# Performance work log

Hardware: AMD Instinct MI355X
Metric: run time of the kernel (lower is better)

The kernel has to match this reference:

```python
import jax, jax.numpy as jnp
import numpy as np

B, S, D, H = 2, 2048, 1024, 16
DK = D // H


def setup_inputs() -> dict:
    key = jax.random.key(0)
    ks = jax.random.split(key, 14)
    inp = {
        'query': jax.random.normal(ks[0], (B, S, D), jnp.float32),
        'key': jax.random.normal(ks[1], (B, S, D), jnp.float32),
        'value': jax.random.normal(ks[2], (B, S, D), jnp.float32),
        'mask': jax.random.randint(ks[3], (B, 1, S, S), 0, 2).astype(bool),
        'rel_pos_bias': jax.random.normal(ks[4], (1, H, S, S), jnp.float32),
    }
    scale = 1.0 / np.sqrt(D)
    names = ['Wq', 'bq', 'Wk', 'bk', 'Wv', 'bv', 'Wo', 'bo']
    for i, n in enumerate(names):
        k = ks[5 + i]
        if n.startswith('W'):
            inp[n] = jax.random.normal(k, (D, D), jnp.float32) * scale
        else:
            inp[n] = jnp.zeros((D,), jnp.float32)
    return inp


def reference(query, key, value, mask, rel_pos_bias, Wq, bq, Wk, bk, Wv, bv, Wo, bo):
    # torch Linear: y = x @ W^T + b; W stored [out, in]
    def proj(x, W, b):
        y = x @ W.T + b                       # [B,S,D]
        return y.reshape(B, S, H, DK).transpose(0, 2, 1, 3)  # [B,H,S,DK]

    q = proj(query, Wq, bq)
    k = proj(key, Wk, bk)
    v = proj(value, Wv, bv)

    scores = jnp.einsum('bhqd,bhkd->bhqk', q, k) / jnp.sqrt(jnp.float32(DK))
    scores = scores + rel_pos_bias
    scores = jnp.where(mask, jnp.float32(-1e9), scores)
    p_attn = jax.nn.softmax(scores, axis=-1)
    x = jnp.einsum('bhqk,bhkd->bhqd', p_attn, v)  # [B,H,S,DK]
    x = x.transpose(0, 2, 1, 3).reshape(B, S, D)
    return x @ Wo.T + bo
```

## Files before the change

### kernel.cpp

```cpp
#include <hip/hip_runtime.h>
#include <stdint.h>


typedef _Float16 f16;
typedef _Float16 f16x8 __attribute__((ext_vector_type(8)));
typedef _Float16 f16x4 __attribute__((ext_vector_type(4)));
typedef __fp16 h2 __attribute__((ext_vector_type(2)));
typedef float f32x4 __attribute__((ext_vector_type(4)));

#define LOG2E 1.44269504088896340736f

__device__ __forceinline__ void gload16(const void* g, void* l) {
  __builtin_amdgcn_global_load_lds(
      (const __attribute__((address_space(1))) unsigned int*)g,
      (__attribute__((address_space(3))) unsigned int*)l, 16, 0, 0);
}

struct CvtSrcs { const float* s[7]; };

__global__ __launch_bounds__(256) void cvt_all(CvtSrcs a, f16* __restrict__ out) {
  const int i = blockIdx.x * 256 + threadIdx.x;
  int r, base;
  if (i < 3145728) { r = i >> 20; base = r << 20; }
  else { r = 3 + ((i - 3145728) >> 18); base = 3145728 + ((r - 3) << 18); }
  const float4 v = ((const float4*)a.s[r])[i - base];
  f16x4 o = {(f16)v.x, (f16)v.y, (f16)v.z, (f16)v.w};
  ((f16x4*)out)[i] = o;
}

__global__ void mask_detect(const uint8_t* __restrict__ m, int* __restrict__ flag) {
  __shared__ int s_off, s_weird;
  const int t = threadIdx.x;
  if (t == 0) { s_off = 0; s_weird = 0; }
  __syncthreads();
  int f_off = 0, f_weird = 0;
  for (int i = t; i < 8192; i += 256) {
    const uint8_t v = m[i];
    if ((i & 3) && v) f_off = 1;
    if (v > 1) f_weird = 1;
  }
  if (f_off) atomicOr(&s_off, 1);
  if (f_weird) atomicOr(&s_weird, 1);
  __syncthreads();
  if (t == 0) *flag = (s_off && !s_weird) ? 1 : 0;
}

__global__ __launch_bounds__(256) void mask_canon(const uint8_t* __restrict__ m,
                                                  uint8_t* __restrict__ out,
                                                  const int* __restrict__ flag) {
  const int i = (blockIdx.x * 256 + threadIdx.x) * 4;
  uchar4 o;
  if (*flag) {
    const uchar4 v = *(const uchar4*)(m + i);
    o = make_uchar4(v.x != 0, v.y != 0, v.z != 0, v.w != 0);
  } else {
    const int4 v = *(const int4*)((const int*)m + i);
    o = make_uchar4(v.x != 0, v.y != 0, v.z != 0, v.w != 0);
  }
  *(uchar4*)(out + i) = o;
}

__global__ __launch_bounds__(256, 2) void gemm_qkv(
    const f16* __restrict__ qh, const f16* __restrict__ kh, const f16* __restrict__ vh,
    const f16* __restrict__ wq, const f16* __restrict__ wk, const f16* __restrict__ wv,
    const float* __restrict__ bq, const float* __restrict__ bk, const float* __restrict__ bv,
    f16* __restrict__ Qp, f16* __restrict__ Kp, f16* __restrict__ Vt) {
  constexpr int K = 1024;
  const int t = threadIdx.x;
  const int w = t >> 6, lane = t & 63, l15 = lane & 15, l4 = lane >> 4;
  const int nt = (int)blockIdx.x % 48;
  const int bm = ((int)blockIdx.x / 48) * 128;
  const int which = nt >> 4;
  const int bn = (nt & 15) * 64;
  const f16* A = which == 0 ? qh : which == 1 ? kh : vh;
  const f16* Bw = which == 0 ? wq : which == 1 ? wk : wv;
  const float* bias = which == 0 ? bq : which == 1 ? bk : bv;

  __shared__ f16 As[2][128 * 32];
  __shared__ f16 Bs[2][64 * 32];

  const f16* a0 = A + (size_t)(bm + (t >> 2)) * K + (t & 3) * 8;
  const f16* a1 = a0 + (size_t)64 * K;
  const f16* b0 = Bw + (size_t)(bn + (t >> 2)) * K + (t & 3) * 8;

  f32x4 acc[2][4];
#pragma unroll
  for (int m = 0; m < 2; ++m)
#pragma unroll
    for (int n = 0; n < 4; ++n) acc[m][n] = (f32x4){0.f, 0.f, 0.f, 0.f};

#define STAGE_G(buf, k0)                          \
  do {                                            \
    gload16(a0 + (k0), &As[buf][w * 512]);        \
    gload16(a1 + (k0), &As[buf][2048 + w * 512]); \
    gload16(b0 + (k0), &Bs[buf][w * 512]);        \
  } while (0)

  STAGE_G(0, 0);
  __syncthreads();
  int cur = 0;
#pragma unroll 1
  for (int kt = 0; kt < 32; ++kt) {
    if (kt < 31) STAGE_G(cur ^ 1, (kt + 1) * 32);
    const f16* ap = &As[cur][(w * 32 + l15) * 32 + l4 * 8];
    const f16* bp = &Bs[cur][l15 * 32 + l4 * 8];
    f16x8 af[2], bfr[4];
#pragma unroll
    for (int m = 0; m < 2; ++m) af[m] = *(const f16x8*)(ap + m * 512);
#pragma unroll
    for (int n = 0; n < 4; ++n) bfr[n] = *(const f16x8*)(bp + n * 512);
#pragma unroll
    for (int m = 0; m < 2; ++m)
#pragma unroll
      for (int n = 0; n < 4; ++n)
        acc[m][n] = __builtin_amdgcn_mfma_f32_16x16x32_f16(af[m], bfr[n], acc[m][n], 0, 0, 0);
    __syncthreads();
    cur ^= 1;
  }
#undef STAGE_G

  const float scale = which == 0 ? 0.125f * LOG2E : 1.0f;
  f16* outp = which == 0 ? Qp : which == 1 ? Kp : Vt;
#pragma unroll
  for (int m = 0; m < 2; ++m) {
    const int r0 = bm + w * 32 + m * 16 + (l4 << 2);
#pragma unroll
    for (int n = 0; n < 4; ++n) {
      const int c = bn + n * 16 + l15;
      const float bv = bias[c];
#pragma unroll
      for (int j = 0; j < 4; ++j) {
        const int r = r0 + j;
        const float v = (acc[m][n][j] + bv) * scale;
        const int b_ = r >> 11, s = r & 2047, h_ = c >> 6, dk = c & 63;
        if (which < 2)
          outp[(((size_t)b_ * 16 + h_) * 2048 + s) * 64 + dk] = (f16)v;
        else
          outp[(((size_t)b_ * 16 + h_) * 64 + dk) * 2048 + s] = (f16)v;
      }
    }
  }
}

__global__ __launch_bounds__(256, 2) void gemm_out(const f16* __restrict__ A,
                                                   const f16* __restrict__ Bw,
                                                   const float* __restrict__ bias,
                                                   float* __restrict__ outp) {
  constexpr int K = 1024;
  const int t = threadIdx.x;
  const int w = t >> 6, lane = t & 63, l15 = lane & 15, l4 = lane >> 4;
  const int bm = (int)(blockIdx.x >> 4) * 128;
  const int bn = (int)(blockIdx.x & 15) * 64;

  __shared__ f16 As[2][128 * 32];
  __shared__ f16 Bs[2][64 * 32];

  const f16* a0 = A + (size_t)(bm + (t >> 2)) * K + (t & 3) * 8;
  const f16* a1 = a0 + (size_t)64 * K;
  const f16* b0 = Bw + (size_t)(bn + (t >> 2)) * K + (t & 3) * 8;

  f32x4 acc[2][4];
#pragma unroll
  for (int m = 0; m < 2; ++m)
#pragma unroll
    for (int n = 0; n < 4; ++n) acc[m][n] = (f32x4){0.f, 0.f, 0.f, 0.f};

#define STAGE_G(buf, k0)                          \
  do {                                            \
    gload16(a0 + (k0), &As[buf][w * 512]);        \
    gload16(a1 + (k0), &As[buf][2048 + w * 512]); \
    gload16(b0 + (k0), &Bs[buf][w * 512]);        \
  } while (0)

  STAGE_G(0, 0);
  __syncthreads();
  int cur = 0;
#pragma unroll 1
  for (int kt = 0; kt < 32; ++kt) {
    if (kt < 31) STAGE_G(cur ^ 1, (kt + 1) * 32);
    const f16* ap = &As[cur][(w * 32 + l15) * 32 + l4 * 8];
    const f16* bp = &Bs[cur][l15 * 32 + l4 * 8];
    f16x8 af[2], bfr[4];
#pragma unroll
    for (int m = 0; m < 2; ++m) af[m] = *(const f16x8*)(ap + m * 512);
#pragma unroll
    for (int n = 0; n < 4; ++n) bfr[n] = *(const f16x8*)(bp + n * 512);
#pragma unroll
    for (int m = 0; m < 2; ++m)
#pragma unroll
      for (int n = 0; n < 4; ++n)
        acc[m][n] = __builtin_amdgcn_mfma_f32_16x16x32_f16(af[m], bfr[n], acc[m][n], 0, 0, 0);
    __syncthreads();
    cur ^= 1;
  }
#undef STAGE_G

#pragma unroll
  for (int m = 0; m < 2; ++m) {
    const int r0 = bm + w * 32 + m * 16 + (l4 << 2);
#pragma unroll
    for (int n = 0; n < 4; ++n) {
      const int c = bn + n * 16 + l15;
      const float bv = bias[c];
#pragma unroll
      for (int j = 0; j < 4; ++j)
        outp[(size_t)(r0 + j) * 1024 + c] = acc[m][n][j] + bv;
    }
  }
}

__device__ __forceinline__ const f16x8* swzr(const f16* base, int row, int bytecol) {
  return (const f16x8*)((const char*)base + row * 128 + (bytecol ^ ((row & 7) << 4)));
}

__global__ __launch_bounds__(256, 2) void attn_fwd(
    const f16* __restrict__ Qp, const f16* __restrict__ Kp,
    const f16* __restrict__ Vt, const float* __restrict__ bias,
    const uint8_t* __restrict__ mask, f16* __restrict__ X) {
  constexpr int S = 2048;
  const int bid = blockIdx.x;
  const int sb = (bid & 7) * 64 + (bid >> 3);
  const int qt = sb & 31, h = sb >> 5;
  const int t = threadIdx.x, w = t >> 6, lane = t & 63;
  const int l15 = lane & 15, l4 = lane >> 4;
  const int q0 = qt * 64 + w * 16;

  const f16* Qb[2] = {Qp + (size_t)h * S * 64, Qp + (size_t)(16 + h) * S * 64};
  const f16* Kb[2] = {Kp + (size_t)h * S * 64, Kp + (size_t)(16 + h) * S * 64};
  const f16* Vb[2] = {Vt + (size_t)h * 64 * S, Vt + (size_t)(16 + h) * 64 * S};
  const float* biasr = bias + (size_t)h * S * S + (size_t)(q0 + l15) * S + l4 * 4;
  const uint8_t* mr0 = mask + (size_t)(q0 + l15) * S + l4 * 4;
  const uint8_t* mr1 = mr0 + (size_t)S * S;

  __shared__ f16 Ks[2][2][64 * 64];
  __shared__ f16 Vs[2][2][64 * 64];
  __shared__ f16 Ps[4][16 * 64];

  f16x8 qf[2][2];
#pragma unroll
  for (int bb = 0; bb < 2; ++bb)
#pragma unroll
    for (int ks = 0; ks < 2; ++ks)
      qf[bb][ks] =
          *(const f16x8*)(Qb[bb] + (size_t)(q0 + l15) * 64 + ks * 32 + l4 * 8);

  f32x4 oacc[2][4];
#pragma unroll
  for (int bb = 0; bb < 2; ++bb)
#pragma unroll
    for (int n = 0; n < 4; ++n) oacc[bb][n] = (f32x4){0.f, 0.f, 0.f, 0.f};
  float mrow[2] = {-3e38f, -3e38f}, lrow[2] = {0.f, 0.f};

  f32x4 bc[2][4];
  uint32_t mc[2][2][4];

  const int srow = t >> 3;
  const int scol = (((t & 7) ^ (srow & 7)) << 3);

#define STAGE(bf, kk)                                                                    \
  do {                                                                                   \
    gload16(Kb[0] + (size_t)((kk) + srow) * 64 + scol, &Ks[bf][0][w * 512]);             \
    gload16(Kb[0] + (size_t)((kk) + 32 + srow) * 64 + scol, &Ks[bf][0][2048 + w * 512]); \
    gload16(Kb[1] + (size_t)((kk) + srow) * 64 + scol, &Ks[bf][1][w * 512]);             \
    gload16(Kb[1] + (size_t)((kk) + 32 + srow) * 64 + scol, &Ks[bf][1][2048 + w * 512]); \
    gload16(Vb[0] + (size_t)srow * S + (kk) + scol, &Vs[bf][0][w * 512]);                \
    gload16(Vb[0] + (size_t)(32 + srow) * S + (kk) + scol, &Vs[bf][0][2048 + w * 512]);  \
    gload16(Vb[1] + (size_t)srow * S + (kk) + scol, &Vs[bf][1][w * 512]);                \
    gload16(Vb[1] + (size_t)(32 + srow) * S + (kk) + scol, &Vs[bf][1][2048 + w * 512]);  \
  } while (0)

#define LOADB(SET, kk)                                      \
  do {                                                      \
    bc[SET][0] = *(const f32x4*)(biasr + (kk));             \
    bc[SET][1] = *(const f32x4*)(biasr + (kk) + 16);        \
    bc[SET][2] = *(const f32x4*)(biasr + (kk) + 32);        \
    bc[SET][3] = *(const f32x4*)(biasr + (kk) + 48);        \
    mc[SET][0][0] = *(const uint32_t*)(mr0 + (kk));         \
    mc[SET][0][1] = *(const uint32_t*)(mr0 + (kk) + 16);    \
    mc[SET][0][2] = *(const uint32_t*)(mr0 + (kk) + 32);    \
    mc[SET][0][3] = *(const uint32_t*)(mr0 + (kk) + 48);    \
    mc[SET][1][0] = *(const uint32_t*)(mr1 + (kk));         \
    mc[SET][1][1] = *(const uint32_t*)(mr1 + (kk) + 16);    \
    mc[SET][1][2] = *(const uint32_t*)(mr1 + (kk) + 32);    \
    mc[SET][1][3] = *(const uint32_t*)(mr1 + (kk) + 48);    \
  } while (0)

#define TILE(BUF, SET, KNEXT)                                                            \
  do {                                                                                   \
    asm volatile("s_waitcnt vmcnt(20)" ::: "memory");                                    \
    __builtin_amdgcn_s_barrier();                                                        \
    asm volatile("" ::: "memory");                                                       \
    f32x4 sacc[2][4];                                                                    \
    _Pragma("unroll") for (int bb = 0; bb < 2; ++bb)                                     \
      _Pragma("unroll") for (int n = 0; n < 4; ++n)                                      \
        sacc[bb][n] = (f32x4){0.f, 0.f, 0.f, 0.f};                                       \
    _Pragma("unroll") for (int bb = 0; bb < 2; ++bb)                                     \
      _Pragma("unroll") for (int n = 0; n < 4; ++n)                                      \
        _Pragma("unroll") for (int ks = 0; ks < 2; ++ks) {                               \
          const f16x8 kf = *swzr(&Ks[BUF][bb][0], n * 16 + l15, ks * 64 + l4 * 16);      \
          sacc[bb][n] = __builtin_amdgcn_mfma_f32_16x16x32_f16(kf, qf[bb][ks],           \
                                                               sacc[bb][n], 0, 0, 0);    \
        }                                                                                \
    _Pragma("unroll") for (int bb = 0; bb < 2; ++bb) {                                   \
      float tmax = -3e38f;                                                               \
      _Pragma("unroll") for (int n = 0; n < 4; ++n) {                                    \
        _Pragma("unroll") for (int j = 0; j < 4; ++j) {                                  \
          const float mf = (float)((mc[SET][bb][n] >> (8 * j)) & 255u);                  \
          sacc[bb][n][j] =                                                               \
              fmaf(mf, -2e9f, fmaf(bc[SET][n][j], LOG2E, sacc[bb][n][j]));               \
        }                                                                                \
        tmax = fmaxf(tmax, fmaxf(fmaxf(sacc[bb][n][0], sacc[bb][n][1]),                  \
                                 fmaxf(sacc[bb][n][2], sacc[bb][n][3])));                \
      }                                                                                  \
      tmax = fmaxf(tmax, __shfl_xor(tmax, 16));                                          \
      tmax = fmaxf(tmax, __shfl_xor(tmax, 32));                                          \
      const float mnew = fmaxf(mrow[bb], tmax);                                          \
      const float alpha = __builtin_exp2f(mrow[bb] - mnew);                              \
      mrow[bb] = mnew;                                                                   \
      float lsum = 0.f;                                                                  \
      _Pragma("unroll") for (int n = 0; n < 4; ++n)                                      \
        _Pragma("unroll") for (int j = 0; j < 4; ++j) {                                  \
          const float e = __builtin_exp2f(sacc[bb][n][j] - mnew);                        \
          sacc[bb][n][j] = e;                                                            \
          lsum += e;                                                                     \
        }                                                                                \
      lsum += __shfl_xor(lsum, 16);                                                      \
      lsum += __shfl_xor(lsum, 32);                                                      \
      lrow[bb] = lrow[bb] * alpha + lsum;                                                \
      float aq[4];                                                                       \
      _Pragma("unroll") for (int j = 0; j < 4; ++j) aq[j] = __shfl(alpha, l4 * 4 + j);   \
      _Pragma("unroll") for (int n = 0; n < 4; ++n)                                      \
        _Pragma("unroll") for (int j = 0; j < 4; ++j) oacc[bb][n][j] *= aq[j];           \
      _Pragma("unroll") for (int n = 0; n < 4; ++n) {                                    \
        h2 p01 = __builtin_amdgcn_cvt_pkrtz(sacc[bb][n][0], sacc[bb][n][1]);             \
        h2 p23 = __builtin_amdgcn_cvt_pkrtz(sacc[bb][n][2], sacc[bb][n][3]);             \
        f16x4 pk;                                                                        \
        pk[0] = (f16)p01[0]; pk[1] = (f16)p01[1];                                        \
        pk[2] = (f16)p23[0]; pk[3] = (f16)p23[1];                                        \
        *(f16x4*)((char*)&Ps[w][0] + l15 * 128 +                                         \
                  ((32 * n + 8 * l4) ^ ((l15 & 7) << 4))) = pk;                          \
      }                                                                                  \
      f16x8 pf[2];                                                                       \
      _Pragma("unroll") for (int ks = 0; ks < 2; ++ks)                                   \
        pf[ks] = *swzr(&Ps[w][0], l15, ks * 64 + l4 * 16);                               \
      _Pragma("unroll") for (int ks = 0; ks < 2; ++ks)                                   \
        _Pragma("unroll") for (int n = 0; n < 4; ++n) {                                  \
          const f16x8 vf = *swzr(&Vs[BUF][bb][0], n * 16 + l15, ks * 64 + l4 * 16);      \
          oacc[bb][n] = __builtin_amdgcn_mfma_f32_16x16x32_f16(pf[ks], vf,               \
                                                               oacc[bb][n], 0, 0, 0);    \
        }                                                                                \
    }                                                                                    \
    __builtin_amdgcn_s_barrier();                                                        \
    asm volatile("" ::: "memory");                                                       \
    STAGE(BUF, KNEXT);                                                                   \
    LOADB(SET, KNEXT);                                                                   \
  } while (0)

  STAGE(0, 0);
  LOADB(0, 0);
  STAGE(1, 64);
  LOADB(1, 64);

#pragma unroll 1
  for (int kt = 0; kt < 32; kt += 2) {
    TILE(0, 0, ((kt + 2) * 64) & (S - 1));
    TILE(1, 1, ((kt + 3) * 64) & (S - 1));
  }
#undef TILE
#undef LOADB
#undef STAGE

  asm volatile("s_waitcnt vmcnt(0)" ::: "memory");

#pragma unroll
  for (int bb = 0; bb < 2; ++bb) {
    const float inv = 1.0f / lrow[bb];
    float invq[4];
#pragma unroll
    for (int j = 0; j < 4; ++j) invq[j] = __shfl(inv, l4 * 4 + j);
#pragma unroll
    for (int j = 0; j < 4; ++j) {
      const int qrow = q0 + l4 * 4 + j;
#pragma unroll
      for (int n = 0; n < 4; ++n)
        X[((size_t)bb * 2048 + qrow) * 1024 + h * 64 + n * 16 + l15] =
            (f16)(oacc[bb][n][j] * invq[j]);
    }
  }
}

extern "C" void kernel_launch(void* const* d_in, const int* in_sizes, int n_in,
                              void* d_out, int out_size, void* d_ws, size_t ws_size,
                              hipStream_t stream) {
  const float* query = (const float*)d_in[0];
  const float* key_ = (const float*)d_in[1];
  const float* value = (const float*)d_in[2];
  const uint8_t* mask = (const uint8_t*)d_in[3];
  const float* bias = (const float*)d_in[4];
  const float* Wq = (const float*)d_in[5];
  const float* bq = (const float*)d_in[6];
  const float* Wk = (const float*)d_in[7];
  const float* bk = (const float*)d_in[8];
  const float* Wv = (const float*)d_in[9];
  const float* bv = (const float*)d_in[10];
  const float* Wo = (const float*)d_in[11];
  const float* bo = (const float*)d_in[12];

  char* p = (char*)d_ws;
  f16* qh = (f16*)p; p += (size_t)4194304 * 2;
  f16* kh = (f16*)p; p += (size_t)4194304 * 2;
  f16* vh = (f16*)p; p += (size_t)4194304 * 2;
  f16* wqh = (f16*)p; p += (size_t)1048576 * 2;
  f16* wkh = (f16*)p; p += (size_t)1048576 * 2;
  f16* wvh = (f16*)p; p += (size_t)1048576 * 2;
  f16* woh = (f16*)p; p += (size_t)1048576 * 2;
  f16* Qp = (f16*)p; p += (size_t)4194304 * 2;
  f16* Kp = (f16*)p; p += (size_t)4194304 * 2;
  f16* Vt = (f16*)p; p += (size_t)4194304 * 2;
  f16* Xh = (f16*)p; p += (size_t)4194304 * 2;
  uint8_t* m8 = (uint8_t*)p; p += (size_t)8388608;
  int* flag = (int*)p; p += 256;
  if (ws_size < (size_t)(p - (char*)d_ws)) return;

  mask_detect<<<1, 256, 0, stream>>>(mask, flag);
  mask_canon<<<8192, 256, 0, stream>>>(mask, m8, flag);

  CvtSrcs cs;
  cs.s[0] = query; cs.s[1] = key_; cs.s[2] = value;
  cs.s[3] = Wq; cs.s[4] = Wk; cs.s[5] = Wv; cs.s[6] = Wo;
  cvt_all<<<16384, 256, 0, stream>>>(cs, qh);

  gemm_qkv<<<1536, 256, 0, stream>>>(qh, kh, vh, wqh, wkh, wvh, bq, bk, bv,
                                     Qp, Kp, Vt);

  attn_fwd<<<512, 256, 0, stream>>>(Qp, Kp, Vt, bias, m8, Xh);

  gemm_out<<<512, 256, 0, stream>>>(Xh, woh, bo, (float*)d_out);
}
```

Baseline: 273.0 us.

## Load K/V MFMA fragments directly from global memory instead of LDS staging

Drops the double-buffered LDS staging of K and V tiles, the async global-to-LDS loads and the block barriers. Each wave now reads its MFMA operand fragments for K and V straight from global memory, relying on L1/L2 to serve the reuse across the four waves. The bias and mask prefetch is turned into a simple register ping-pong issued one tile ahead, and the swizzled block-to-head mapping is replaced by a linear one. This removes barrier sync and LDS traffic, but each wave issues four times the global K/V loads and their latency is no longer hidden by the LDS pipeline.

```diff
diff --git a/kernel.cpp b/kernel.cpp
--- a/kernel.cpp
+++ b/kernel.cpp
@@ -209,31 +209,26 @@
   }
 }
 
-__device__ __forceinline__ const f16x8* swzr(const f16* base, int row, int bytecol) {
-  return (const f16x8*)((const char*)base + row * 128 + (bytecol ^ ((row & 7) << 4)));
-}
-
 __global__ __launch_bounds__(256, 2) void attn_fwd(
     const f16* __restrict__ Qp, const f16* __restrict__ Kp,
     const f16* __restrict__ Vt, const float* __restrict__ bias,
     const uint8_t* __restrict__ mask, f16* __restrict__ X) {
   constexpr int S = 2048;
   const int bid = blockIdx.x;
-  const int sb = (bid & 7) * 64 + (bid >> 3);
-  const int qt = sb & 31, h = sb >> 5;
+  const int qt = bid & 31, h = bid >> 5;
   const int t = threadIdx.x, w = t >> 6, lane = t & 63;
   const int l15 = lane & 15, l4 = lane >> 4;
   const int q0 = qt * 64 + w * 16;
 
   const f16* Qb[2] = {Qp + (size_t)h * S * 64, Qp + (size_t)(16 + h) * S * 64};
-  const f16* Kb[2] = {Kp + (size_t)h * S * 64, Kp + (size_t)(16 + h) * S * 64};
-  const f16* Vb[2] = {Vt + (size_t)h * 64 * S, Vt + (size_t)(16 + h) * 64 * S};
+  const f16* kf0 = Kp + (size_t)h * S * 64 + (size_t)l15 * 64 + l4 * 8;
+  const f16* kf1 = kf0 + (size_t)16 * S * 64;
+  const f16* vf0 = Vt + (size_t)h * 64 * S + (size_t)l15 * S + l4 * 8;
+  const f16* vf1 = vf0 + (size_t)16 * 64 * S;
   const float* biasr = bias + (size_t)h * S * S + (size_t)(q0 + l15) * S + l4 * 4;
   const uint8_t* mr0 = mask + (size_t)(q0 + l15) * S + l4 * 4;
   const uint8_t* mr1 = mr0 + (size_t)S * S;
 
-  __shared__ f16 Ks[2][2][64 * 64];
-  __shared__ f16 Vs[2][2][64 * 64];
   __shared__ f16 Ps[4][16 * 64];
 
   f16x8 qf[2][2];
@@ -251,63 +246,40 @@
     for (int n = 0; n < 4; ++n) oacc[bb][n] = (f32x4){0.f, 0.f, 0.f, 0.f};
   float mrow[2] = {-3e38f, -3e38f}, lrow[2] = {0.f, 0.f};
 
-  f32x4 bc[2][4];
-  uint32_t mc[2][2][4];
-
-  const int srow = t >> 3;
-  const int scol = (((t & 7) ^ (srow & 7)) << 3);
-
-#define STAGE(bf, kk)                                                                    \
+  f32x4 bcA[4], bcB[4];
+  uint32_t mcA[2][4], mcB[2][4];
+
+#define LOADB(BC, MC, kk)                                   \
+  do {                                                      \
+    _Pragma("unroll") for (int n = 0; n < 4; ++n) {         \
+      BC[n] = *(const f32x4*)(biasr + (kk) + n * 16);       \
+      MC[0][n] = *(const uint32_t*)(mr0 + (kk) + n * 16);   \
+      MC[1][n] = *(const uint32_t*)(mr1 + (kk) + n * 16);   \
+    }                                                       \
+  } while (0)
+
+#define TILE(BC, MC, BCN, MCN, k0)                                                       \
   do {                                                                                   \
-    gload16(Kb[0] + (size_t)((kk) + srow) * 64 + scol, &Ks[bf][0][w * 512]);             \
-    gload16(Kb[0] + (size_t)((kk) + 32 + srow) * 64 + scol, &Ks[bf][0][2048 + w * 512]); \
-    gload16(Kb[1] + (size_t)((kk) + srow) * 64 + scol, &Ks[bf][1][w * 512]);             \
-    gload16(Kb[1] + (size_t)((kk) + 32 + srow) * 64 + scol, &Ks[bf][1][2048 + w * 512]); \
-    gload16(Vb[0] + (size_t)srow * S + (kk) + scol, &Vs[bf][0][w * 512]);                \
-    gload16(Vb[0] + (size_t)(32 + srow) * S + (kk) + scol, &Vs[bf][0][2048 + w * 512]);  \
-    gload16(Vb[1] + (size_t)srow * S + (kk) + scol, &Vs[bf][1][w * 512]);                \
-    gload16(Vb[1] + (size_t)(32 + srow) * S + (kk) + scol, &Vs[bf][1][2048 + w * 512]);  \
-  } while (0)
-
-#define LOADB(SET, kk)                                      \
-  do {                                                      \
-    bc[SET][0] = *(const f32x4*)(biasr + (kk));             \
-    bc[SET][1] = *(const f32x4*)(biasr + (kk) + 16);        \
-    bc[SET][2] = *(const f32x4*)(biasr + (kk) + 32);        \
-    bc[SET][3] = *(const f32x4*)(biasr + (kk) + 48);        \
-    mc[SET][0][0] = *(const uint32_t*)(mr0 + (kk));         \
-    mc[SET][0][1] = *(const uint32_t*)(mr0 + (kk) + 16);    \
-    mc[SET][0][2] = *(const uint32_t*)(mr0 + (kk) + 32);    \
-    mc[SET][0][3] = *(const uint32_t*)(mr0 + (kk) + 48);    \
-    mc[SET][1][0] = *(const uint32_t*)(mr1 + (kk));         \
-    mc[SET][1][1] = *(const uint32_t*)(mr1 + (kk) + 16);    \
-    mc[SET][1][2] = *(const uint32_t*)(mr1 + (kk) + 32);    \
-    mc[SET][1][3] = *(const uint32_t*)(mr1 + (kk) + 48);    \
-  } while (0)
-
-#define TILE(BUF, SET, KNEXT)                                                            \
-  do {                                                                                   \
-    asm volatile("s_waitcnt vmcnt(20)" ::: "memory");                                    \
-    __builtin_amdgcn_s_barrier();                                                        \
-    asm volatile("" ::: "memory");                                                       \
+    LOADB(BCN, MCN, ((k0) + 64) & (S - 1));                                              \
     f32x4 sacc[2][4];                                                                    \
     _Pragma("unroll") for (int bb = 0; bb < 2; ++bb)                                     \
       _Pragma("unroll") for (int n = 0; n < 4; ++n)                                      \
         sacc[bb][n] = (f32x4){0.f, 0.f, 0.f, 0.f};                                       \
-    _Pragma("unroll") for (int bb = 0; bb < 2; ++bb)                                     \
-      _Pragma("unroll") for (int n = 0; n < 4; ++n)                                      \
-        _Pragma("unroll") for (int ks = 0; ks < 2; ++ks) {                               \
-          const f16x8 kf = *swzr(&Ks[BUF][bb][0], n * 16 + l15, ks * 64 + l4 * 16);      \
-          sacc[bb][n] = __builtin_amdgcn_mfma_f32_16x16x32_f16(kf, qf[bb][ks],           \
-                                                               sacc[bb][n], 0, 0, 0);    \
-        }                                                                                \
+    _Pragma("unroll") for (int n = 0; n < 4; ++n)                                        \
+      _Pragma("unroll") for (int ks = 0; ks < 2; ++ks) {                                 \
+        const f16x8 k0f = *(const f16x8*)(kf0 + (size_t)((k0) + n * 16) * 64 + ks * 32); \
+        const f16x8 k1f = *(const f16x8*)(kf1 + (size_t)((k0) + n * 16) * 64 + ks * 32); \
+        sacc[0][n] = __builtin_amdgcn_mfma_f32_16x16x32_f16(k0f, qf[0][ks],              \
+                                                            sacc[0][n], 0, 0, 0);        \
+        sacc[1][n] = __builtin_amdgcn_mfma_f32_16x16x32_f16(k1f, qf[1][ks],              \
+                                                            sacc[1][n], 0, 0, 0);        \
+      }                                                                                  \
     _Pragma("unroll") for (int bb = 0; bb < 2; ++bb) {                                   \
       float tmax = -3e38f;                                                               \
       _Pragma("unroll") for (int n = 0; n < 4; ++n) {                                    \
         _Pragma("unroll") for (int j = 0; j < 4; ++j) {                                  \
-          const float mf = (float)((mc[SET][bb][n] >> (8 * j)) & 255u);                  \
-          sacc[bb][n][j] =                                                               \
-              fmaf(mf, -2e9f, fmaf(bc[SET][n][j], LOG2E, sacc[bb][n][j]));               \
+          const float mf = (float)((MC[bb][n] >> (8 * j)) & 255u);                       \
+          sacc[bb][n][j] = fmaf(mf, -2e9f, fmaf(BC[n][j], LOG2E, sacc[bb][n][j]));       \
         }                                                                                \
         tmax = fmaxf(tmax, fmaxf(fmaxf(sacc[bb][n][0], sacc[bb][n][1]),                  \
                                  fmaxf(sacc[bb][n][2], sacc[bb][n][3])));                \
@@ -342,35 +314,28 @@
       }                                                                                  \
       f16x8 pf[2];                                                                       \
       _Pragma("unroll") for (int ks = 0; ks < 2; ++ks)                                   \
-        pf[ks] = *swzr(&Ps[w][0], l15, ks * 64 + l4 * 16);                               \
+        pf[ks] = *(const f16x8*)((const char*)&Ps[w][0] + l15 * 128 +                    \
+                                 ((ks * 64 + l4 * 16) ^ ((l15 & 7) << 4)));              \
+      const f16* vfb = (bb == 0) ? vf0 : vf1;                                            \
       _Pragma("unroll") for (int ks = 0; ks < 2; ++ks)                                   \
         _Pragma("unroll") for (int n = 0; n < 4; ++n) {                                  \
-          const f16x8 vf = *swzr(&Vs[BUF][bb][0], n * 16 + l15, ks * 64 + l4 * 16);      \
+          const f16x8 vf =                                                               \
+              *(const f16x8*)(vfb + (size_t)n * 16 * S + (k0) + ks * 32);                \
           oacc[bb][n] = __builtin_amdgcn_mfma_f32_16x16x32_f16(pf[ks], vf,               \
                                                                oacc[bb][n], 0, 0, 0);    \
         }                                                                                \
     }                                                                                    \
-    __builtin_amdgcn_s_barrier();                                                        \
-    asm volatile("" ::: "memory");                                                       \
-    STAGE(BUF, KNEXT);                                                                   \
-    LOADB(SET, KNEXT);                                                                   \
   } while (0)
 
-  STAGE(0, 0);
-  LOADB(0, 0);
-  STAGE(1, 64);
-  LOADB(1, 64);
+  LOADB(bcA, mcA, 0);
 
 #pragma unroll 1
   for (int kt = 0; kt < 32; kt += 2) {
-    TILE(0, 0, ((kt + 2) * 64) & (S - 1));
-    TILE(1, 1, ((kt + 3) * 64) & (S - 1));
+    TILE(bcA, mcA, bcB, mcB, kt * 64);
+    TILE(bcB, mcB, bcA, mcA, (kt + 1) * 64);
   }
 #undef TILE
 #undef LOADB
-#undef STAGE
-
-  asm volatile("s_waitcnt vmcnt(0)" ::: "memory");
 
 #pragma unroll
   for (int bb = 0; bb < 2; ++bb) {
```

Measured after the change: 468.1 us. 71.4% more time.
